# Performance work log

Measured on AMD Instinct MI355X. Metric: run time of the kernel, lower is better.

## Reference

```python
import jax, jax.numpy as jnp
import numpy as np

B, C, H, W = 8, 256, 48, 48
QC = C // 8                # query/key channels
MIP = max(8, C // 32)      # CoordAtt bottleneck channels
EPS = 1e-5                 # BatchNorm eps (inference, running_mean=0, running_var=1)


def _conv1x1(x, Wt, b=None):
    # 1x1 conv == channel matmul: x [b,c,h,w], Wt [o,c]
    y = jnp.einsum('bchw,oc->bohw', x, Wt)
    if b is not None:
        y = y + b[None, :, None, None]
    return y


def _bn(x, w, b):
    # inference BatchNorm with running_mean=0, running_var=1
    s = w * np.float32(1.0 / np.sqrt(1.0 + EPS))
    return x * s[None, :, None, None] + b[None, :, None, None]


def setup_inputs() -> dict:
    key = jax.random.key(0)
    ks = jax.random.split(key, 22)
    r = lambda k, sh, s=0.05: jax.random.normal(k, sh, jnp.float32) * s
    return dict(
        f1=jax.random.normal(ks[0], (B, C, H, W), jnp.float32),
        f2=jax.random.normal(ks[1], (B, C, H, W), jnp.float32),
        t1=r(ks[2], (1, C, 1, 1), 1.0),
        t2=r(ks[3], (1, C, 1, 1), 1.0),
        Wq=r(ks[4], (QC, C)), bq=r(ks[5], (QC,)),
        Wk=r(ks[6], (QC, C)), bk=r(ks[7], (QC,)),
        Wv=r(ks[8], (C, C)), bv=r(ks[9], (C,)),
        gamma=jnp.full((1,), 0.5, jnp.float32),
        ca_w1=r(ks[10], (MIP, C)), ca_b1=r(ks[11], (MIP,)),
        ca_bn_w=1.0 + r(ks[12], (MIP,)), ca_bn_b=r(ks[13], (MIP,)),
        ca_wh=r(ks[14], (C, MIP)), ca_bh=r(ks[15], (C,)),
        ca_ww=r(ks[16], (C, MIP)), ca_bw=r(ks[17], (C,)),
        fus_w=r(ks[18], (C, 2 * C)),
        fus_bn_w=1.0 + r(ks[19], (C,)), fus_bn_b=r(ks[20], (C,)),
    )


def _cross_attention(f1, f2, t1, t2, Wq, bq, Wk, bk, Wv, bv, gamma):
    b, c, h, w = f1.shape
    N = h * w
    f1e = f1 + t1
    f2e = f2 + t2

    def qkv(fe):
        q = _conv1x1(fe, Wq, bq).reshape(b, QC, N).transpose(0, 2, 1)  # [b,N,qc]
        k = _conv1x1(fe, Wk, bk).reshape(b, QC, N)                     # [b,qc,N]
        v = _conv1x1(fe, Wv, bv).reshape(b, c, N)                      # [b,c,N]
        return q, k, v

    q1, k1, v1 = qkv(f1e)
    q2, k2, v2 = qkv(f2e)

    # CrossAtt_1 = softmax(Q2 @ K1^T) applied to V1
    attn21 = jax.nn.softmax(jnp.einsum('bmq,bqn->bmn', q2, k1), axis=-1)  # [b,N,N]
    out1 = jnp.einsum('bcn,bmn->bcm', v1, attn21).reshape(b, c, h, w)
    # CrossAtt_2 = softmax(Q1 @ K2^T) applied to V2
    attn12 = jax.nn.softmax(jnp.einsum('bmq,bqn->bmn', q1, k2), axis=-1)
    out2 = jnp.einsum('bcn,bmn->bcm', v2, attn12).reshape(b, c, h, w)

    return gamma[0] * out1 + f1, gamma[0] * out2 + f2


def _coord_att(x, w1, b1, bnw, bnb, wh, bh, ww, bw):
    b, c, h, w = x.shape
    x_h = jnp.mean(x, axis=3, keepdims=True)                         # [b,c,h,1]
    x_w = jnp.mean(x, axis=2, keepdims=True).transpose(0, 1, 3, 2)   # [b,c,w,1]
    y = jnp.concatenate([x_h, x_w], axis=2)                          # [b,c,h+w,1]
    y = jax.nn.relu(_bn(_conv1x1(y, w1, b1), bnw, bnb))
    yh, yw = y[:, :, :h], y[:, :, h:]
    a_h = jax.nn.sigmoid(_conv1x1(yh, wh, bh))                       # [b,c,h,1]
    a_w = jax.nn.sigmoid(_conv1x1(yw.transpose(0, 1, 3, 2), ww, bw)) # [b,c,1,w]
    return x * a_w * a_h


def _fusion(x, Wf, bnw, bnb):
    return jax.nn.relu(_bn(_conv1x1(x, Wf), bnw, bnb))


def reference(f1, f2, t1, t2, Wq, bq, Wk, bk, Wv, bv, gamma,
              ca_w1, ca_b1, ca_bn_w, ca_bn_b, ca_wh, ca_bh, ca_ww, ca_bw,
              fus_w, fus_bn_w, fus_bn_b):
    a1, a2 = _cross_attention(f1, f2, t1, t2, Wq, bq, Wk, bk, Wv, bv, gamma)
    c1 = _coord_att(f1, ca_w1, ca_b1, ca_bn_w, ca_bn_b, ca_wh, ca_bh, ca_ww, ca_bw)
    c2 = _coord_att(f2, ca_w1, ca_b1, ca_bn_w, ca_bn_b, ca_wh, ca_bh, ca_ww, ca_bw)
    o1 = _fusion(jnp.concatenate([a1, c1], axis=1), fus_w, fus_bn_w, fus_bn_b)
    o2 = _fusion(jnp.concatenate([a2, c2], axis=1), fus_w, fus_bn_w, fus_bn_b)
    return o1, o2
```

## Files before the change

kernel.cpp:

```cpp
#include <hip/hip_runtime.h>
#include <hip/hip_bf16.h>

typedef unsigned short ushort_t;
typedef __attribute__((ext_vector_type(8))) short short8;
typedef __attribute__((ext_vector_type(4))) float floatx4;
typedef __attribute__((ext_vector_type(16))) float floatx16;
typedef __attribute__((ext_vector_type(4))) unsigned int uintx4;


__device__ __forceinline__ float bf2f(ushort_t u) {
    return __uint_as_float(((unsigned int)u) << 16);
}
__device__ __forceinline__ ushort_t f2bf(float f) {
    unsigned int x = __float_as_uint(f);
    unsigned int r = (x + 0x7fffu + ((x >> 16) & 1u)) >> 16;
    return (ushort_t)r;
}
__device__ __forceinline__ unsigned int pkbf(float a, float b) {
    __hip_bfloat162 h = __float22bfloat162_rn(float2{a, b});
    return *reinterpret_cast<unsigned int*>(&h);
}
__device__ __forceinline__ float loadIn(const void* p, size_t i, int isbf) {
    return isbf ? bf2f(((const ushort_t*)p)[i]) : ((const float*)p)[i];
}
__device__ __forceinline__ float fexp2(float x) {
#if __has_builtin(__builtin_amdgcn_exp2f)
    return __builtin_amdgcn_exp2f(x);
#else
    return exp2f(x);
#endif
}
__device__ __forceinline__ void plswap(unsigned& a, unsigned& b, int h) {
#if __has_builtin(__builtin_amdgcn_permlane32_swap)
    auto r = __builtin_amdgcn_permlane32_swap(a, b, false, false);
    a = r[0];
    b = r[1];
#else
    unsigned sa = __shfl_xor(a, 32), sb = __shfl_xor(b, 32);
    unsigned na = (h == 0) ? a : sb;
    unsigned nb = (h == 0) ? sa : b;
    a = na; b = nb;
#endif
}

#define BN_SCALE 0.9999950000374997f
#define LOG2E    1.4426950408889634f
#define ZERO16 (floatx16){0.f,0.f,0.f,0.f,0.f,0.f,0.f,0.f,0.f,0.f,0.f,0.f,0.f,0.f,0.f,0.f}

#define P_T1    0
#define P_T2    256
#define P_WQ    512
#define P_BQ    8704
#define P_WK    8768
#define P_BK    16960
#define P_WV    17024
#define P_BV    82560
#define P_GAMMA 82624
#define P_CAW1  82688
#define P_CAB1  84736
#define P_BNW   84800
#define P_BNB   84864
#define P_WH    84928
#define P_BH    86976
#define P_WW    87232
#define P_BW    89280
#define P_FUSW  89536
#define P_FBNW  220608
#define P_FBNB  220864
#define P_BQ2   221120

__global__ void detect_kernel(const void* gamma, int* flag) {
    if (threadIdx.x == 0) {
        ushort_t u = ((const ushort_t*)gamma)[0];
        *flag = (u != 0) ? 1 : 0;
    }
}

__global__ __launch_bounds__(256) void convert_params(
    const void* t1, const void* t2, const void* Wq, const void* bq,
    const void* Wk, const void* bk, const void* Wv, const void* bv,
    const void* gm, const void* cw1, const void* cb1, const void* bnw,
    const void* bnb, const void* wh, const void* bh, const void* ww,
    const void* bw, const void* fw, const void* fbnw, const void* fbnb,
    const int* flagp, float* dst, ushort_t* WA, ushort_t* WF)
{
    int isbf = *flagp;
    const void* srcs[20] = {t1,t2,Wq,bq,Wk,bk,Wv,bv,gm,cw1,cb1,bnw,bnb,wh,bh,ww,bw,fw,fbnw,fbnb};
    const int   cnts[20] = {256,256,8192,32,8192,32,65536,256,1,2048,8,8,8,2048,256,2048,256,131072,256,256};
    const int   offs[20] = {P_T1,P_T2,P_WQ,P_BQ,P_WK,P_BK,P_WV,P_BV,P_GAMMA,P_CAW1,P_CAB1,
                            P_BNW,P_BNB,P_WH,P_BH,P_WW,P_BW,P_FUSW,P_FBNW,P_FBNB};
    int tid = blockIdx.x * 256 + threadIdx.x;
    int stride = gridDim.x * 256;
    #pragma unroll
    for (int sg = 0; sg < 20; sg++) {
        float* d = dst + offs[sg];
        for (int i = tid; i < cnts[sg]; i += stride) d[i] = loadIn(srcs[sg], i, isbf);
    }
    for (int i = tid; i < 81920; i += stride) {
        int o = i >> 8, c = i & 255;
        float v;
        if (o < 32)      v = loadIn(Wq, o * 256 + c, isbf);
        else if (o < 64) v = loadIn(Wk, (o - 32) * 256 + c, isbf);
        else             v = loadIn(Wv, (size_t)(o - 64) * 256 + c, isbf);
        WA[i] = f2bf(v);
    }
    for (int i = tid; i < 131072; i += stride) WF[i] = f2bf(loadIn(fw, i, isbf));
    int gw = tid >> 6, lane = tid & 63;
    if (gw < 640) {
        int side = gw / 320, o = gw % 320;
        const void* tsrc = side ? t2 : t1;
        float bias; const void* Wsrc; size_t wbase;
        if (o < 32)      { bias = loadIn(bq, o, isbf);       Wsrc = Wq; wbase = (size_t)o * 256; }
        else if (o < 64) { bias = loadIn(bk, o - 32, isbf);  Wsrc = Wk; wbase = (size_t)(o - 32) * 256; }
        else             { bias = loadIn(bv, o - 64, isbf);  Wsrc = Wv; wbase = (size_t)(o - 64) * 256; }
        float s = 0.f;
        for (int c = lane; c < 256; c += 64) s += loadIn(Wsrc, wbase + c, isbf) * loadIn(tsrc, c, isbf);
        s += __shfl_xor(s, 1);  s += __shfl_xor(s, 2);  s += __shfl_xor(s, 4);
        s += __shfl_xor(s, 8);  s += __shfl_xor(s, 16); s += __shfl_xor(s, 32);
        if (lane == 0) dst[P_BQ2 + gw] = bias + s;
    }
}

__global__ __launch_bounds__(256) void prep1_kernel(
    const void* __restrict__ f1, const void* __restrict__ f2,
    const int* __restrict__ flagp, ushort_t* __restrict__ fT)
{
    __shared__ ushort_t tr[64][264];
    int isbf = *flagp;
    int blk = blockIdx.x;
    int nt = blk % 36, sb = blk / 36;
    int side = sb >> 3, b = sb & 7;
    int n0 = nt * 64;
    const void* f = side ? f2 : f1;
    int t = threadIdx.x;
    size_t base = ((size_t)b * 256 + t) * 2304 + n0;
    if (isbf) {
        const ushort_t* fp = (const ushort_t*)f + base;
        #pragma unroll
        for (int i = 0; i < 8; i++) {
            uint4 raw = *(const uint4*)&fp[i * 8];
            const ushort_t* rp = (const ushort_t*)&raw;
            #pragma unroll
            for (int j = 0; j < 8; j++) tr[i * 8 + j][t] = rp[j];
        }
    } else {
        const float* fp = (const float*)f + base;
        #pragma unroll
        for (int i = 0; i < 16; i++) {
            float4 raw = *(const float4*)&fp[i * 4];
            unsigned u0 = pkbf(raw.x, raw.y), u1 = pkbf(raw.z, raw.w);
            tr[i * 4 + 0][t] = (ushort_t)u0;
            tr[i * 4 + 1][t] = (ushort_t)(u0 >> 16);
            tr[i * 4 + 2][t] = (ushort_t)u1;
            tr[i * 4 + 3][t] = (ushort_t)(u1 >> 16);
        }
    }
    __syncthreads();
    #pragma unroll
    for (int i = 0; i < 8; i++) {
        int chunk = i * 256 + t;
        int row = chunk >> 5, k8 = (chunk & 31) * 8;
        *(uint4*)&fT[((size_t)sb * 2304 + n0 + row) * 256 + k8] = *(const uint4*)&tr[row][k8];
    }
}

__global__ __launch_bounds__(256) void qkv_gemm(
    const ushort_t* __restrict__ fT, const ushort_t* __restrict__ WA,
    const float* __restrict__ P,
    ushort_t* __restrict__ qG, ushort_t* __restrict__ kG, ushort_t* __restrict__ vG)
{
    __shared__ ushort_t xs[64][264];
    int blk = blockIdx.x;
    int nt = blk % 36, sb = blk / 36;
    int side = sb >> 3;
    int n0 = nt * 64;
    int t = threadIdx.x;
    int w = t >> 6, l = t & 63, q = l >> 4, ln = l & 15;
    #pragma unroll
    for (int i = 0; i < 8; i++) {
        int chunk = i * 256 + t;
        int row = chunk >> 5, k8 = (chunk & 31) * 8;
        *(uint4*)&xs[row][k8] = *(const uint4*)&fT[((size_t)sb * 2304 + n0 + row) * 256 + k8];
    }
    __syncthreads();
    floatx4 acc[5][4];
    #pragma unroll
    for (int mi = 0; mi < 5; mi++)
        #pragma unroll
        for (int ns = 0; ns < 4; ns++) acc[mi][ns] = (floatx4){0.f, 0.f, 0.f, 0.f};
    #pragma unroll
    for (int ks = 0; ks < 8; ks++) {
        short8 a[5];
        #pragma unroll
        for (int mi = 0; mi < 5; mi++)
            a[mi] = *(const short8*)&WA[(size_t)(w * 80 + mi * 16 + ln) * 256 + ks * 32 + q * 8];
        #pragma unroll
        for (int ns = 0; ns < 4; ns++) {
            short8 bfr = *(const short8*)&xs[ns * 16 + ln][ks * 32 + q * 8];
            #pragma unroll
            for (int mi = 0; mi < 5; mi++)
                acc[mi][ns] = __builtin_amdgcn_mfma_f32_16x16x32_bf16(a[mi], bfr, acc[mi][ns], 0, 0, 0);
        }
    }
    const float* bp = P + P_BQ2 + side * 320;
    #pragma unroll
    for (int mi = 0; mi < 5; mi++) {
        int o0 = w * 80 + mi * 16 + q * 4;
        #pragma unroll
        for (int ns = 0; ns < 4; ns++) {
            int n = n0 + ns * 16 + ln;
            if (o0 < 32) {
                uint2 pk;
                pk.x = pkbf((acc[mi][ns][0] + bp[o0]) * LOG2E, (acc[mi][ns][1] + bp[o0 + 1]) * LOG2E);
                pk.y = pkbf((acc[mi][ns][2] + bp[o0 + 2]) * LOG2E, (acc[mi][ns][3] + bp[o0 + 3]) * LOG2E);
                *(uint2*)&qG[((size_t)sb * 2304 + n) * 32 + o0] = pk;
            } else if (o0 < 64) {
                uint2 pk;
                pk.x = pkbf(acc[mi][ns][0] + bp[o0], acc[mi][ns][1] + bp[o0 + 1]);
                pk.y = pkbf(acc[mi][ns][2] + bp[o0 + 2], acc[mi][ns][3] + bp[o0 + 3]);
                *(uint2*)&kG[((size_t)sb * 2304 + n) * 32 + (o0 - 32)] = pk;
            } else {
                unsigned u0 = pkbf(acc[mi][ns][0] + bp[o0], acc[mi][ns][1] + bp[o0 + 1]);
                unsigned u1 = pkbf(acc[mi][ns][2] + bp[o0 + 2], acc[mi][ns][3] + bp[o0 + 3]);
                vG[((size_t)sb * 256 + (o0 - 64 + 0)) * 2304 + n] = (ushort_t)u0;
                vG[((size_t)sb * 256 + (o0 - 64 + 1)) * 2304 + n] = (ushort_t)(u0 >> 16);
                vG[((size_t)sb * 256 + (o0 - 64 + 2)) * 2304 + n] = (ushort_t)u1;
                vG[((size_t)sb * 256 + (o0 - 64 + 3)) * 2304 + n] = (ushort_t)(u1 >> 16);
            }
        }
    }
}

__global__ __launch_bounds__(256) void pool_kernel(
    const ushort_t* __restrict__ fT, float* __restrict__ pools)
{
    int blk = blockIdx.x;
    int j = blk % 96, sb = blk / 96;
    int c = threadIdx.x;
    const ushort_t* base = fT + (size_t)sb * 2304 * 256 + c;
    float s = 0.f;
    if (j < 48) {
        int h = j;
        #pragma unroll 8
        for (int w = 0; w < 48; w++) s += bf2f(base[(size_t)(h * 48 + w) * 256]);
    } else {
        int w = j - 48;
        #pragma unroll 8
        for (int h = 0; h < 48; h++) s += bf2f(base[(size_t)(h * 48 + w) * 256]);
    }
    pools[(size_t)sb * 24576 + c * 96 + j] = s * (1.f / 48.f);
}

__global__ __launch_bounds__(256) void coord_kernel(
    const float* __restrict__ pools, const float* __restrict__ P,
    float* __restrict__ attv)
{
    __shared__ float w1s[8][256];
    __shared__ float ys[8][96];
    int sb = blockIdx.x;
    int t = threadIdx.x;
    for (int ff = t; ff < 2048; ff += 256) w1s[ff >> 8][ff & 255] = P[P_CAW1 + ff];
    __syncthreads();
    const float* pin = pools + (size_t)sb * 24576;
    if (t < 96) {
        float s[8];
        #pragma unroll
        for (int mp = 0; mp < 8; mp++) s[mp] = 0.f;
        for (int c = 0; c < 256; c++) {
            float p = pin[c * 96 + t];
            #pragma unroll
            for (int mp = 0; mp < 8; mp++) s[mp] += w1s[mp][c] * p;
        }
        #pragma unroll
        for (int mp = 0; mp < 8; mp++) {
            float vv = s[mp] + P[P_CAB1 + mp];
            vv = vv * (P[P_BNW + mp] * BN_SCALE) + P[P_BNB + mp];
            ys[mp][t] = fmaxf(vv, 0.f);
        }
    }
    __syncthreads();
    float* aout = attv + (size_t)sb * 24576;
    for (int ff = t; ff < 24576; ff += 256) {
        int j = ff >> 8, c = ff & 255;
        const float* W = P + ((j < 48) ? P_WH : P_WW);
        const float* B = P + ((j < 48) ? P_BH : P_BW);
        float s = B[c];
        #pragma unroll
        for (int mp = 0; mp < 8; mp++) s += W[c * 8 + mp] * ys[mp][j];
        aout[ff] = 1.f / (1.f + __expf(-s));
    }
}

__global__ __launch_bounds__(256) void attn_kernel(
    const ushort_t* __restrict__ qG, const ushort_t* __restrict__ kG,
    const ushort_t* __restrict__ vG,
    ushort_t* __restrict__ O0, ushort_t* __restrict__ O1,
    float* __restrict__ lbuf)
{
    __shared__ ushort_t smem[18432];
    __shared__ float lred[4][32];

    int i = blockIdx.x;
    int xcd = i & 7, slot = i >> 3;
    int dhi = (slot >= 72) ? 1 : 0;
    int db = xcd + (dhi << 3);
    int rem = slot - 72 * dhi;
    int sp = rem & 1, mt = rem >> 1;
    int qsb = db ^ 8;

    int t = threadIdx.x;
    int w = t >> 6;
    int qsw = w & 1, ksw = w >> 1;
    int cseg = w;
    int l = t & 63, r31 = l & 31, h = l >> 5;
    int q0 = mt * 64, c0 = cseg * 64;

    short8 qf0, qf1;
    {
        const ushort_t* qrow = qG + ((size_t)qsb * 2304 + q0 + qsw * 32 + r31) * 32;
        qf0 = *(const short8*)&qrow[h * 8];
        qf1 = *(const short8*)&qrow[16 + h * 8];
    }

    const ushort_t* kW = kG + ((size_t)db * 2304 + ksw * 32 + r31) * 32 + h * 8;
    const ushort_t* vbase = vG + ((size_t)db * 256 + c0) * 2304;

    floatx16 o[2][2];
    #pragma unroll
    for (int qs = 0; qs < 2; qs++)
        #pragma unroll
        for (int cs = 0; cs < 2; cs++) o[qs][cs] = ZERO16;
    float l_lane = 0.f;

    int nstart = sp * 1152;
    for (int tile = 0; tile < 18; tile++) {
        int n0 = nstart + tile * 64;
        int buf = tile & 1;
        short8 k0 = *(const short8*)&kW[(size_t)n0 * 32];
        short8 k1 = *(const short8*)&kW[(size_t)n0 * 32 + 16];
        floatx16 s = ZERO16;
        s = __builtin_amdgcn_mfma_f32_32x32x16_bf16(k0, qf0, s, 0, 0, 0);
        s = __builtin_amdgcn_mfma_f32_32x32x16_bf16(k1, qf1, s, 0, 0, 0);
        float e[16];
        #pragma unroll
        for (int r = 0; r < 16; r++) e[r] = fexp2(s[r]);
        l_lane += (((e[0] + e[1]) + (e[2] + e[3])) + ((e[4] + e[5]) + (e[6] + e[7])))
                + (((e[8] + e[9]) + (e[10] + e[11])) + ((e[12] + e[13]) + (e[14] + e[15])));
        unsigned wd[8];
        #pragma unroll
        for (int p2 = 0; p2 < 8; p2++) wd[p2] = pkbf(e[2 * p2], e[2 * p2 + 1]);
        plswap(wd[0], wd[2], h); plswap(wd[1], wd[3], h);
        plswap(wd[4], wd[6], h); plswap(wd[5], wd[7], h);
        uintx4 A0 = {wd[0], wd[1], wd[2], wd[3]};
        uintx4 A1 = {wd[4], wd[5], wd[6], wd[7]};
        *(uintx4*)&smem[(size_t)(((buf * 2 + qsw) * 4 + ksw * 2 + 0) * 64 + l) * 8] = A0;
        *(uintx4*)&smem[(size_t)(((buf * 2 + qsw) * 4 + ksw * 2 + 1) * 64 + l) * 8] = A1;
        __syncthreads();
        #pragma unroll
        for (int kt = 0; kt < 4; kt++) {
            short8 af0 = *(const short8*)&smem[(size_t)(((buf * 2 + 0) * 4 + kt) * 64 + l) * 8];
            short8 af1 = *(const short8*)&smem[(size_t)(((buf * 2 + 1) * 4 + kt) * 64 + l) * 8];
            #pragma unroll
            for (int cs = 0; cs < 2; cs++) {
                short8 vf = *(const short8*)&vbase[(size_t)(cs * 32 + r31) * 2304 + n0 + kt * 16 + h * 8];
                o[0][cs] = __builtin_amdgcn_mfma_f32_32x32x16_bf16(af0, vf, o[0][cs], 0, 0, 0);
                o[1][cs] = __builtin_amdgcn_mfma_f32_32x32x16_bf16(af1, vf, o[1][cs], 0, 0, 0);
            }
        }
    }
    float lt = l_lane + __shfl_xor(l_lane, 32);
    __syncthreads();
    lred[w][r31] = lt;
    ushort_t* ow = &smem[(size_t)w * 64 * 72];
    #pragma unroll
    for (int qs = 0; qs < 2; qs++) {
        #pragma unroll
        for (int cs = 0; cs < 2; cs++) {
            #pragma unroll
            for (int r = 0; r < 16; r++) {
                int qloc = qs * 32 + (r & 3) + 8 * (r >> 2) + 4 * h;
                ow[qloc * 72 + cs * 32 + r31] = f2bf(o[qs][cs][r]);
            }
        }
    }
    __syncthreads();
    ushort_t* Op = sp ? O1 : O0;
    size_t obase = ((size_t)db * 2304 + q0) * 256 + c0;
    int rrow8 = l >> 3, rch0 = (l & 7) * 8;
    #pragma unroll
    for (int pass = 0; pass < 8; pass++) {
        int row = pass * 8 + rrow8;
        uintx4 v = *(const uintx4*)&ow[row * 72 + rch0];
        __builtin_nontemporal_store(v, (uintx4*)&Op[obase + (size_t)row * 256 + rch0]);
    }
    if (t < 64) {
        int base = ((db * 36 + mt) * 2 + sp) * 64;
        int qs = t >> 5, r = t & 31;
        lbuf[base + t] = lred[qs][r] + lred[qs + 2][r];
    }
}

__global__ __launch_bounds__(256) void fusion_gemm(
    const ushort_t* __restrict__ O0, const ushort_t* __restrict__ O1,
    const ushort_t* __restrict__ fT, const float* __restrict__ attv,
    const float* __restrict__ lbuf,
    const ushort_t* __restrict__ WF, const float* __restrict__ P,
    const int* __restrict__ flagp, void* __restrict__ dout)
{
    __shared__ ushort_t xs[64][264];
    __shared__ float sS[64];
    int isbf = *flagp;
    int blk = blockIdx.x;
    int nt = blk % 36, sb = blk / 36;
    int n0 = nt * 64;
    int t = threadIdx.x;
    int w = t >> 6, l = t & 63, q = l >> 4, ln = l & 15;
    if (t < 64) {
        float l0 = lbuf[(sb * 36 + nt) * 128 + t];
        float l1 = lbuf[(sb * 36 + nt) * 128 + 64 + t];
        sS[t] = P[P_GAMMA] / (l0 + l1);
    }
    __syncthreads();
    floatx4 acc[4][4];
    #pragma unroll
    for (int ms = 0; ms < 4; ms++)
        #pragma unroll
        for (int ns = 0; ns < 4; ns++) acc[ms][ns] = (floatx4){0.f, 0.f, 0.f, 0.f};
    size_t tbase = ((size_t)sb * 2304 + n0) * 256;
    #pragma unroll
    for (int i = 0; i < 8; i++) {
        int chunk = i * 256 + t;
        int row = chunk >> 5, k8 = (chunk & 31) * 8;
        size_t idx = tbase + (size_t)row * 256 + k8;
        uintx4 u0 = __builtin_nontemporal_load((const uintx4*)&O0[idx]);
        uintx4 u1 = __builtin_nontemporal_load((const uintx4*)&O1[idx]);
        uint4 uf = *(const uint4*)&fT[idx];
        const ushort_t* a0 = (const ushort_t*)&u0;
        const ushort_t* a1 = (const ushort_t*)&u1;
        const ushort_t* ff = (const ushort_t*)&uf;
        float s = sS[row];
        float v[8];
        #pragma unroll
        for (int j = 0; j < 8; j++) v[j] = (bf2f(a0[j]) + bf2f(a1[j])) * s + bf2f(ff[j]);
        uint4 pk;
        pk.x = pkbf(v[0], v[1]); pk.y = pkbf(v[2], v[3]);
        pk.z = pkbf(v[4], v[5]); pk.w = pkbf(v[6], v[7]);
        *(uint4*)&xs[row][k8] = pk;
    }
    __syncthreads();
    #pragma unroll
    for (int ks = 0; ks < 8; ks++) {
        short8 a[4];
        #pragma unroll
        for (int ms = 0; ms < 4; ms++)
            a[ms] = *(const short8*)&WF[(size_t)(w * 64 + ms * 16 + ln) * 512 + ks * 32 + q * 8];
        #pragma unroll
        for (int ns = 0; ns < 4; ns++) {
            short8 bfr = *(const short8*)&xs[ns * 16 + ln][ks * 32 + q * 8];
            #pragma unroll
            for (int ms = 0; ms < 4; ms++)
                acc[ms][ns] = __builtin_amdgcn_mfma_f32_16x16x32_bf16(a[ms], bfr, acc[ms][ns], 0, 0, 0);
        }
    }
    __syncthreads();
    const float* av = attv + (size_t)sb * 24576;
    #pragma unroll
    for (int i = 0; i < 8; i++) {
        int chunk = i * 256 + t;
        int row = chunk >> 5, k8 = (chunk & 31) * 8;
        int n = n0 + row;
        int h = n / 48, ww2 = n - h * 48;
        size_t idx = tbase + (size_t)row * 256 + k8;
        uint4 uf = *(const uint4*)&fT[idx];
        const ushort_t* ff = (const ushort_t*)&uf;
        float ah[8], aw[8];
        *(float4*)&ah[0] = *(const float4*)&av[h * 256 + k8];
        *(float4*)&ah[4] = *(const float4*)&av[h * 256 + k8 + 4];
        *(float4*)&aw[0] = *(const float4*)&av[(48 + ww2) * 256 + k8];
        *(float4*)&aw[4] = *(const float4*)&av[(48 + ww2) * 256 + k8 + 4];
        float v[8];
        #pragma unroll
        for (int j = 0; j < 8; j++) v[j] = bf2f(ff[j]) * ah[j] * aw[j];
        uint4 pk;
        pk.x = pkbf(v[0], v[1]); pk.y = pkbf(v[2], v[3]);
        pk.z = pkbf(v[4], v[5]); pk.w = pkbf(v[6], v[7]);
        *(uint4*)&xs[row][k8] = pk;
    }
    __syncthreads();
    #pragma unroll
    for (int ks = 0; ks < 8; ks++) {
        short8 a[4];
        #pragma unroll
        for (int ms = 0; ms < 4; ms++)
            a[ms] = *(const short8*)&WF[(size_t)(w * 64 + ms * 16 + ln) * 512 + 256 + ks * 32 + q * 8];
        #pragma unroll
        for (int ns = 0; ns < 4; ns++) {
            short8 bfr = *(const short8*)&xs[ns * 16 + ln][ks * 32 + q * 8];
            #pragma unroll
            for (int ms = 0; ms < 4; ms++)
                acc[ms][ns] = __builtin_amdgcn_mfma_f32_16x16x32_bf16(a[ms], bfr, acc[ms][ns], 0, 0, 0);
        }
    }
    #pragma unroll
    for (int ms = 0; ms < 4; ms++) {
        int o0 = w * 64 + ms * 16 + q * 4;
        float bw[4], bb[4];
        #pragma unroll
        for (int r = 0; r < 4; r++) {
            bw[r] = P[P_FBNW + o0 + r] * BN_SCALE;
            bb[r] = P[P_FBNB + o0 + r];
        }
        #pragma unroll
        for (int ns = 0; ns < 4; ns++) {
            int n = n0 + ns * 16 + ln;
            #pragma unroll
            for (int r = 0; r < 4; r++) {
                float v = acc[ms][ns][r] * bw[r] + bb[r];
                v = (v < 0.f) ? 0.f : v;
                size_t oidx = (size_t)sb * 589824 + (size_t)(o0 + r) * 2304 + n;
                if (isbf) ((ushort_t*)dout)[oidx] = f2bf(v);
                else      ((float*)dout)[oidx] = v;
            }
        }
    }
}

extern "C" void kernel_launch(void* const* d_in, const int* in_sizes, int n_in,
                              void* d_out, int out_size, void* d_ws, size_t ws_size,
                              hipStream_t stream) {
    const void* f1 = d_in[0]; const void* f2 = d_in[1];

    char* ws = (char*)d_ws;
    int*      flag  = (int*)(ws + 0);
    float*    P     = (float*)(ws + 1024);
    ushort_t* WA    = (ushort_t*)(ws + 917504);
    ushort_t* WF    = (ushort_t*)(ws + 1081344);
    ushort_t* fT    = (ushort_t*)(ws + 1343488);
    ushort_t* qG    = (ushort_t*)(ws + 20217856);
    ushort_t* kG    = (ushort_t*)(ws + 22577152);
    ushort_t* vG    = (ushort_t*)(ws + 24936448);
    ushort_t* O0    = (ushort_t*)(ws + 43810816);
    float*    pools = (float*)(ws + 62685184);
    float*    attv  = (float*)(ws + 64258048);
    ushort_t* O1    = (ushort_t*)(ws + 65830912);
    float*    lbuf  = pools;

    detect_kernel<<<dim3(1), dim3(64), 0, stream>>>(d_in[10], flag);
    convert_params<<<dim3(160), dim3(256), 0, stream>>>(
        d_in[2], d_in[3], d_in[4], d_in[5], d_in[6], d_in[7], d_in[8], d_in[9],
        d_in[10], d_in[11], d_in[12], d_in[13], d_in[14], d_in[15], d_in[16],
        d_in[17], d_in[18], d_in[19], d_in[20], d_in[21], flag, P, WA, WF);
    prep1_kernel<<<dim3(576), dim3(256), 0, stream>>>(f1, f2, flag, fT);
    qkv_gemm<<<dim3(576), dim3(256), 0, stream>>>(fT, WA, P, qG, kG, vG);
    pool_kernel<<<dim3(1536), dim3(256), 0, stream>>>(fT, pools);
    coord_kernel<<<dim3(16), dim3(256), 0, stream>>>(pools, P, attv);
    attn_kernel<<<dim3(1152), dim3(256), 0, stream>>>(qG, kG, vG, O0, O1, lbuf);
    fusion_gemm<<<dim3(576), dim3(256), 0, stream>>>(
        O0, O1, fT, attv, lbuf, WF, P, flag, d_out);
}
```

Before: 371.5 us.

## Software-pipeline QK^T/exp with PV MFMAs and halve attention LDS footprint

```diff
diff --git a/kernel.cpp b/kernel.cpp
--- a/kernel.cpp
+++ b/kernel.cpp
@@ -297,7 +297,7 @@
     ushort_t* __restrict__ O0, ushort_t* __restrict__ O1,
     float* __restrict__ lbuf)
 {
-    __shared__ ushort_t smem[18432];
+    __shared__ ushort_t smem[9216];
     __shared__ float lred[4][32];
 
     int i = blockIdx.x;
@@ -311,9 +311,8 @@
     int t = threadIdx.x;
     int w = t >> 6;
     int qsw = w & 1, ksw = w >> 1;
-    int cseg = w;
     int l = t & 63, r31 = l & 31, h = l >> 5;
-    int q0 = mt * 64, c0 = cseg * 64;
+    int q0 = mt * 64, c0 = w * 64;
 
     short8 qf0, qf1;
     {
@@ -333,29 +332,44 @@
     float l_lane = 0.f;
 
     int nstart = sp * 1152;
-    for (int tile = 0; tile < 18; tile++) {
+
+#define DO_S_PUBLISH(K0, K1, BUF)                                              \
+    {                                                                          \
+        floatx16 s_ = ZERO16;                                                  \
+        s_ = __builtin_amdgcn_mfma_f32_32x32x16_bf16(K0, qf0, s_, 0, 0, 0);    \
+        s_ = __builtin_amdgcn_mfma_f32_32x32x16_bf16(K1, qf1, s_, 0, 0, 0);    \
+        float e_[16];                                                          \
+        _Pragma("unroll")                                                      \
+        for (int r_ = 0; r_ < 16; r_++) e_[r_] = fexp2(s_[r_]);                \
+        l_lane += (((e_[0] + e_[1]) + (e_[2] + e_[3]))                         \
+                 + ((e_[4] + e_[5]) + (e_[6] + e_[7])))                        \
+                + (((e_[8] + e_[9]) + (e_[10] + e_[11]))                       \
+                 + ((e_[12] + e_[13]) + (e_[14] + e_[15])));                   \
+        unsigned wd_[8];                                                       \
+        _Pragma("unroll")                                                      \
+        for (int p_ = 0; p_ < 8; p_++) wd_[p_] = pkbf(e_[2 * p_], e_[2 * p_ + 1]); \
+        plswap(wd_[0], wd_[2], h); plswap(wd_[1], wd_[3], h);                  \
+        plswap(wd_[4], wd_[6], h); plswap(wd_[5], wd_[7], h);                  \
+        uintx4 A0_ = {wd_[0], wd_[1], wd_[2], wd_[3]};                         \
+        uintx4 A1_ = {wd_[4], wd_[5], wd_[6], wd_[7]};                         \
+        *(uintx4*)&smem[(size_t)((((BUF) * 2 + qsw) * 4 + ksw * 2 + 0) * 64 + l) * 8] = A0_; \
+        *(uintx4*)&smem[(size_t)((((BUF) * 2 + qsw) * 4 + ksw * 2 + 1) * 64 + l) * 8] = A1_; \
+    }
+
+    {
+        const ushort_t* kp = kW + (size_t)nstart * 32;
+        short8 k0 = *(const short8*)&kp[0];
+        short8 k1 = *(const short8*)&kp[16];
+        DO_S_PUBLISH(k0, k1, 0)
+    }
+    __syncthreads();
+
+    for (int tile = 0; tile < 17; tile++) {
         int n0 = nstart + tile * 64;
         int buf = tile & 1;
-        short8 k0 = *(const short8*)&kW[(size_t)n0 * 32];
-        short8 k1 = *(const short8*)&kW[(size_t)n0 * 32 + 16];
-        floatx16 s = ZERO16;
-        s = __builtin_amdgcn_mfma_f32_32x32x16_bf16(k0, qf0, s, 0, 0, 0);
-        s = __builtin_amdgcn_mfma_f32_32x32x16_bf16(k1, qf1, s, 0, 0, 0);
-        float e[16];
-        #pragma unroll
-        for (int r = 0; r < 16; r++) e[r] = fexp2(s[r]);
-        l_lane += (((e[0] + e[1]) + (e[2] + e[3])) + ((e[4] + e[5]) + (e[6] + e[7])))
-                + (((e[8] + e[9]) + (e[10] + e[11])) + ((e[12] + e[13]) + (e[14] + e[15])));
-        unsigned wd[8];
-        #pragma unroll
-        for (int p2 = 0; p2 < 8; p2++) wd[p2] = pkbf(e[2 * p2], e[2 * p2 + 1]);
-        plswap(wd[0], wd[2], h); plswap(wd[1], wd[3], h);
-        plswap(wd[4], wd[6], h); plswap(wd[5], wd[7], h);
-        uintx4 A0 = {wd[0], wd[1], wd[2], wd[3]};
-        uintx4 A1 = {wd[4], wd[5], wd[6], wd[7]};
-        *(uintx4*)&smem[(size_t)(((buf * 2 + qsw) * 4 + ksw * 2 + 0) * 64 + l) * 8] = A0;
-        *(uintx4*)&smem[(size_t)(((buf * 2 + qsw) * 4 + ksw * 2 + 1) * 64 + l) * 8] = A1;
-        __syncthreads();
+        const ushort_t* kp = kW + (size_t)(n0 + 64) * 32;
+        short8 k0n = *(const short8*)&kp[0];
+        short8 k1n = *(const short8*)&kp[16];
         #pragma unroll
         for (int kt = 0; kt < 4; kt++) {
             short8 af0 = *(const short8*)&smem[(size_t)(((buf * 2 + 0) * 4 + kt) * 64 + l) * 8];
@@ -367,32 +381,50 @@
                 o[1][cs] = __builtin_amdgcn_mfma_f32_32x32x16_bf16(af1, vf, o[1][cs], 0, 0, 0);
             }
         }
-    }
+        DO_S_PUBLISH(k0n, k1n, (buf ^ 1))
+        __syncthreads();
+    }
+    {
+        int n0 = nstart + 17 * 64;
+        #pragma unroll
+        for (int kt = 0; kt < 4; kt++) {
+            short8 af0 = *(const short8*)&smem[(size_t)(((1 * 2 + 0) * 4 + kt) * 64 + l) * 8];
+            short8 af1 = *(const short8*)&smem[(size_t)(((1 * 2 + 1) * 4 + kt) * 64 + l) * 8];
+            #pragma unroll
+            for (int cs = 0; cs < 2; cs++) {
+                short8 vf = *(const short8*)&vbase[(size_t)(cs * 32 + r31) * 2304 + n0 + kt * 16 + h * 8];
+                o[0][cs] = __builtin_amdgcn_mfma_f32_32x32x16_bf16(af0, vf, o[0][cs], 0, 0, 0);
+                o[1][cs] = __builtin_amdgcn_mfma_f32_32x32x16_bf16(af1, vf, o[1][cs], 0, 0, 0);
+            }
+        }
+    }
+#undef DO_S_PUBLISH
+
     float lt = l_lane + __shfl_xor(l_lane, 32);
     __syncthreads();
     lred[w][r31] = lt;
-    ushort_t* ow = &smem[(size_t)w * 64 * 72];
+    ushort_t* Op = sp ? O1 : O0;
+    size_t obase = ((size_t)db * 2304 + q0) * 256 + c0;
+    ushort_t* ow = &smem[(size_t)w * 2304];
+    int rrow8 = l >> 3, rch0 = (l & 7) * 8;
     #pragma unroll
     for (int qs = 0; qs < 2; qs++) {
         #pragma unroll
         for (int cs = 0; cs < 2; cs++) {
             #pragma unroll
             for (int r = 0; r < 16; r++) {
-                int qloc = qs * 32 + (r & 3) + 8 * (r >> 2) + 4 * h;
+                int qloc = (r & 3) + 8 * (r >> 2) + 4 * h;
                 ow[qloc * 72 + cs * 32 + r31] = f2bf(o[qs][cs][r]);
             }
         }
-    }
-    __syncthreads();
-    ushort_t* Op = sp ? O1 : O0;
-    size_t obase = ((size_t)db * 2304 + q0) * 256 + c0;
-    int rrow8 = l >> 3, rch0 = (l & 7) * 8;
-    #pragma unroll
-    for (int pass = 0; pass < 8; pass++) {
-        int row = pass * 8 + rrow8;
-        uintx4 v = *(const uintx4*)&ow[row * 72 + rch0];
-        __builtin_nontemporal_store(v, (uintx4*)&Op[obase + (size_t)row * 256 + rch0]);
-    }
+        #pragma unroll
+        for (int pass = 0; pass < 4; pass++) {
+            int row = pass * 8 + rrow8;
+            uintx4 v = *(const uintx4*)&ow[row * 72 + rch0];
+            __builtin_nontemporal_store(v, (uintx4*)&Op[obase + (size_t)(qs * 32 + row) * 256 + rch0]);
+        }
+    }
+    __syncthreads();
     if (t < 64) {
         int base = ((db * 36 + mt) * 2 + sp) * 64;
         int qs = t >> 5, r = t & 31;
```

Result: slower. 389.1 us (+4.7%).
